# Kernel tuning notes

Measured on AMD Instinct MI355X. Metric: run time of the kernel, lower is better.

## Reference

```python
import jax, jax.numpy as jnp
import numpy as np

D_MODEL = 1024
NUM_HEADS = 16
D_INTERNAL = D_MODEL // NUM_HEADS
ROPE_BASE = 10000.0


def justnorm(x):
    return x / jnp.linalg.norm(x, axis=-1, keepdims=True)


def rotate_half(x):
    h = x.shape[-1] // 2
    return jnp.concatenate([-x[..., h:], x[..., :h]], axis=-1)


def setup_inputs() -> dict:
    key = jax.random.key(0)
    ks = jax.random.split(key, 8)
    B, T, dm, H, di = 4, 2048, D_MODEL, NUM_HEADS, D_INTERNAL
    x = jax.random.normal(ks[0], (B, T, dm), dtype=jnp.float32)
    stdev_h = 1.0 / (dm + di) ** 0.5
    qkv = jax.random.uniform(ks[1], (H, 3 * di, dm), minval=-stdev_h, maxval=stdev_h, dtype=jnp.float32)
    qkv = justnorm(qkv)  # per-row L2 normalization as in torch init
    sqk = (dm ** -0.5) * jnp.ones((H, di), dtype=jnp.float32)
    stdev = 1.0 / (4 * dm + dm) ** 0.5
    W_O = justnorm(jax.random.uniform(ks[2], (dm, dm), minval=-stdev, maxval=stdev, dtype=jnp.float32))
    Wu = justnorm(jax.random.uniform(ks[3], (8 * dm, dm), minval=-stdev, maxval=stdev, dtype=jnp.float32))
    Wv = justnorm(jax.random.uniform(ks[4], (dm, 4 * dm), minval=-stdev, maxval=stdev, dtype=jnp.float32))
    attn_alpha = (dm ** -0.5) * jnp.ones((dm,), dtype=jnp.float32)
    mlp_alpha = jnp.ones((dm,), dtype=jnp.float32)
    suv = jnp.ones((8 * dm,), dtype=jnp.float32)
    return {"x": x, "qkv": qkv, "sqk": sqk, "W_O": W_O, "Wu": Wu, "Wv": Wv,
            "attn_alpha": attn_alpha, "mlp_alpha": mlp_alpha, "suv": suv}


def _forward(x, qkv, sqk, W_O, Wu, Wv, attn_alpha, mlp_alpha, suv):
    B, T, dm = x.shape
    H = qkv.shape[0]
    di = qkv.shape[1] // 3
    sqrt_dm = jnp.sqrt(jnp.asarray(dm, x.dtype))
    # Per-head QKV projection, batched over heads: [B,H,T,3*di]
    qkv_out = jnp.einsum('btd,hed->bhte', x, qkv)
    Q, K, V = jnp.split(qkv_out, 3, axis=-1)
    # RoPE over full d_internal
    inv_freq = 1.0 / (ROPE_BASE ** (jnp.arange(0, di, 2, dtype=jnp.float32) / di))
    freqs = jnp.arange(T, dtype=jnp.float32)[:, None] * inv_freq[None, :]
    emb = jnp.concatenate([freqs, freqs], axis=-1)  # [T, di]
    cos, sin = jnp.cos(emb), jnp.sin(emb)
    Q = Q * cos + rotate_half(Q) * sin
    K = K * cos + rotate_half(K) * sin
    # sqk effective scale: sqk * (1.0 / d_model**-0.5)
    sqk_eff = sqk * sqrt_dm  # [H, di]
    Q = justnorm(Q) * sqk_eff[None, :, None, :]
    K = justnorm(K) * sqk_eff[None, :, None, :]
    # SDPA with non-standard scale = d_model**0.5, causal (eval mode)
    scores = jnp.einsum('bhqd,bhkd->bhqk', Q, K) * sqrt_dm
    causal = jnp.tril(jnp.ones((T, T), dtype=bool))
    scores = jnp.where(causal[None, None], scores, jnp.finfo(x.dtype).min)
    attn = jax.nn.softmax(scores, axis=-1)
    out = jnp.einsum('bhqk,bhkd->bhqd', attn, V)
    t = out.transpose(0, 2, 1, 3).reshape(B, T, dm)
    t = t @ W_O.T
    # nGPT-style attention lerp residual: attn_alpha * (0.05 / d_model**-0.5)
    lr = jnp.abs(attn_alpha * (0.05 * sqrt_dm))
    A = justnorm(x)
    Bn = justnorm(t)
    x1 = justnorm(A + lr * (Bn - A))
    # SwiGLU MLP
    uv = x1 @ Wu.T
    uv = (suv * sqrt_dm) * uv
    tn = justnorm(uv)
    u, v = jnp.split(tn, 2, axis=-1)
    res = u * jax.nn.silu(v)
    t = res @ Wv.T
    lr2 = jnp.abs(mlp_alpha * 0.05)
    A = justnorm(x1)
    Bn = justnorm(t)
    return justnorm(A + lr2 * (Bn - A))


def reference(x, qkv, sqk, W_O, Wu, Wv, attn_alpha, mlp_alpha, suv):
    return _forward(x, qkv, sqk, W_O, Wu, Wv, attn_alpha, mlp_alpha, suv)
```

## Files before the change

### kernel.cpp

```cpp
#include <hip/hip_runtime.h>
#include <hip/hip_bf16.h>


#define B_   4
#define T_   2048
#define DM   1024
#define H_   16
#define DI   64
#define NROW (B_ * T_)

using bf16 = __hip_bfloat16;
typedef __attribute__((ext_vector_type(8))) short bfrag;
typedef __attribute__((ext_vector_type(4))) float f4;

__device__ __forceinline__ void  stf(float* p, float v) { *p = v; }
__device__ __forceinline__ void  stf(bf16* p, float v)  { *p = __float2bfloat16(v); }

__device__ __forceinline__ unsigned short bfbits(float a) {
    bf16 h = __float2bfloat16(a);
    return __builtin_bit_cast(unsigned short, h);
}
__device__ __forceinline__ unsigned pk2(float a, float b) {
    return (unsigned)bfbits(a) | ((unsigned)bfbits(b) << 16);
}

__device__ __forceinline__ float wave_sum(float v) {
#pragma unroll
    for (int off = 32; off; off >>= 1) v += __shfl_xor(v, off, 64);
    return v;
}

__device__ __forceinline__ float block_sum(float v) {
    __shared__ float sm[4];
    int lane = threadIdx.x & 63, w = threadIdx.x >> 6;
    v = wave_sum(v);
    __syncthreads();
    if (lane == 0) sm[w] = v;
    __syncthreads();
    return sm[0] + sm[1] + sm[2] + sm[3];
}

typedef __attribute__((address_space(1))) const void g_void;
typedef __attribute__((address_space(3))) void l_void;
__device__ __forceinline__ void gl_lds(const void* g, void* l) {
    __builtin_amdgcn_global_load_lds((g_void*)g, (l_void*)l, 16, 0, 0);
}

__global__ __launch_bounds__(256)
void f32_to_bf16_k(const float* __restrict__ in, bf16* __restrict__ out, long n)
{
    long i = ((long)blockIdx.x * 256 + threadIdx.x) * 8;
    if (i >= n) return;
    float4 a = *(const float4*)(in + i);
    float4 b = *(const float4*)(in + i + 4);
    union { bfrag f; unsigned u[4]; } o;
    o.u[0] = pk2(a.x, a.y); o.u[1] = pk2(a.z, a.w);
    o.u[2] = pk2(b.x, b.y); o.u[3] = pk2(b.z, b.w);
    *(bfrag*)(out + i) = o.f;
}

template <typename TC>
__global__ __launch_bounds__(256)
void gemm_bf16(const bf16* __restrict__ A, const bf16* __restrict__ Bm,
               TC* __restrict__ C, int M, int N, int K)
{
    __shared__ bf16 lds[2][2][128 * 32];
    const int tid  = threadIdx.x;
    const int w    = tid >> 6, lane = tid & 63;
    const int g    = lane >> 4, c = lane & 15;
    const int m0   = blockIdx.y * 128, n0 = blockIdx.x * 128;
    const int wm   = w >> 1, wn = w & 1;

    const int srow = (lane >> 2);
    const int skc  = 8 * (lane & 3);

    f4 acc[4][4] = {{{0,0,0,0}}};

    const int NT = K >> 5;

#pragma unroll
    for (int q = 0; q < 2; q++) {
        int cidx = w * 2 + q;
        int row  = 16 * cidx + srow;
        gl_lds(A + (long)(m0 + row) * K + skc, &lds[0][0][cidx * 512]);
        gl_lds(Bm + (long)(n0 + row) * K + skc, &lds[0][1][cidx * 512]);
    }
    __syncthreads();

    for (int t = 0; t < NT; t++) {
        int cur = t & 1;
        if (t + 1 < NT) {
            int k0 = (t + 1) << 5;
#pragma unroll
            for (int q = 0; q < 2; q++) {
                int cidx = w * 2 + q;
                int row  = 16 * cidx + srow;
                gl_lds(A + (long)(m0 + row) * K + k0 + skc, &lds[cur ^ 1][0][cidx * 512]);
                gl_lds(Bm + (long)(n0 + row) * K + k0 + skc, &lds[cur ^ 1][1][cidx * 512]);
            }
        }
        const bf16* bufA = &lds[cur][0][0];
        const bf16* bufB = &lds[cur][1][0];
        bfrag af[4], bb[4];
#pragma unroll
        for (int mi = 0; mi < 4; mi++)
            af[mi] = *(const bfrag*)(bufA + (64 * wm + 16 * mi + c) * 32 + 8 * g);
#pragma unroll
        for (int ni = 0; ni < 4; ni++)
            bb[ni] = *(const bfrag*)(bufB + (64 * wn + 16 * ni + c) * 32 + 8 * g);
#pragma unroll
        for (int mi = 0; mi < 4; mi++)
#pragma unroll
            for (int ni = 0; ni < 4; ni++)
                acc[mi][ni] = __builtin_amdgcn_mfma_f32_16x16x32_bf16(
                    af[mi], bb[ni], acc[mi][ni], 0, 0, 0);
        __syncthreads();
    }

#pragma unroll
    for (int mi = 0; mi < 4; mi++)
#pragma unroll
        for (int ni = 0; ni < 4; ni++) {
            long row = m0 + 64 * wm + 16 * mi + 4 * g;
            long col = n0 + 64 * wn + 16 * ni + c;
#pragma unroll
            for (int r = 0; r < 4; r++)
                stf(&C[(row + r) * N + col], acc[mi][ni][r]);
        }
}

template <typename TC>
__global__ __launch_bounds__(512, 2)
void gemm_bf16_256(const bf16* __restrict__ A, const bf16* __restrict__ Bm,
                   TC* __restrict__ C, int M, int N, int K)
{
    __shared__ bf16 lds[2][2][256 * 64];
    const int tid  = threadIdx.x;
    const int w    = tid >> 6, lane = tid & 63;
    const int g    = lane >> 4, c = lane & 15;
    const int m0   = blockIdx.y * 256, n0 = blockIdx.x * 256;
    const int wm   = w & 1, wn = w >> 1;
    const int srow8 = lane >> 3;
    const int swz   = 8 * ((lane & 7) ^ srow8);
    const int cx    = c & 7;

    f4 acc[8][4] = {{{0,0,0,0}}};

    const int NT = K >> 6;

    auto STAGE = [&](int buf, int t) {
        int k0 = t << 6;
#pragma unroll
        for (int i = 0; i < 4; i++) {
            int rb = w * 32 + i * 8;
            gl_lds(A  + (long)(m0 + rb + srow8) * K + k0 + swz, &lds[buf][0][rb * 64]);
            gl_lds(Bm + (long)(n0 + rb + srow8) * K + k0 + swz, &lds[buf][1][rb * 64]);
        }
    };

    STAGE(0, 0);
    STAGE(1, 1);
    asm volatile("s_waitcnt vmcnt(8)" ::: "memory");
    __builtin_amdgcn_s_barrier();

    for (int t = 0; t < NT; t++) {
        const bf16* bufA = &lds[t & 1][0][0];
        const bf16* bufB = &lds[t & 1][1][0];

        bfrag a0[4][2], b0[4][2];
#pragma unroll
        for (int mi = 0; mi < 4; mi++)
#pragma unroll
            for (int kk = 0; kk < 2; kk++)
                a0[mi][kk] = *(const bfrag*)(bufA + (wm * 128 + mi * 16 + c) * 64
                                                  + 8 * ((4 * kk + g) ^ cx));
#pragma unroll
        for (int ni = 0; ni < 4; ni++)
#pragma unroll
            for (int kk = 0; kk < 2; kk++)
                b0[ni][kk] = *(const bfrag*)(bufB + (wn * 64 + ni * 16 + c) * 64
                                                  + 8 * ((4 * kk + g) ^ cx));
        asm volatile("s_waitcnt lgkmcnt(0)" ::: "memory");
        __builtin_amdgcn_sched_barrier(0);
        __builtin_amdgcn_s_setprio(1);
#pragma unroll
        for (int mi = 0; mi < 4; mi++)
#pragma unroll
            for (int ni = 0; ni < 4; ni++) {
                acc[mi][ni] = __builtin_amdgcn_mfma_f32_16x16x32_bf16(
                    a0[mi][0], b0[ni][0], acc[mi][ni], 0, 0, 0);
                acc[mi][ni] = __builtin_amdgcn_mfma_f32_16x16x32_bf16(
                    a0[mi][1], b0[ni][1], acc[mi][ni], 0, 0, 0);
            }
        __builtin_amdgcn_s_setprio(0);

        bfrag a1[4][2];
#pragma unroll
        for (int mi = 0; mi < 4; mi++)
#pragma unroll
            for (int kk = 0; kk < 2; kk++)
                a1[mi][kk] = *(const bfrag*)(bufA + (wm * 128 + (mi + 4) * 16 + c) * 64
                                                  + 8 * ((4 * kk + g) ^ cx));
        asm volatile("s_waitcnt lgkmcnt(0)" ::: "memory");
        __builtin_amdgcn_sched_barrier(0);
        __builtin_amdgcn_s_setprio(1);
#pragma unroll
        for (int mi = 0; mi < 4; mi++)
#pragma unroll
            for (int ni = 0; ni < 4; ni++) {
                acc[mi + 4][ni] = __builtin_amdgcn_mfma_f32_16x16x32_bf16(
                    a1[mi][0], b0[ni][0], acc[mi + 4][ni], 0, 0, 0);
                acc[mi + 4][ni] = __builtin_amdgcn_mfma_f32_16x16x32_bf16(
                    a1[mi][1], b0[ni][1], acc[mi + 4][ni], 0, 0, 0);
            }
        __builtin_amdgcn_s_setprio(0);

        __builtin_amdgcn_s_barrier();
        if (t + 2 < NT) {
            STAGE(t & 1, t + 2);
            asm volatile("s_waitcnt vmcnt(8)" ::: "memory");
        } else if (t + 1 < NT) {
            asm volatile("s_waitcnt vmcnt(0)" ::: "memory");
        }
        __builtin_amdgcn_s_barrier();
    }

#pragma unroll
    for (int mi = 0; mi < 8; mi++)
#pragma unroll
        for (int ni = 0; ni < 4; ni++) {
            long row = m0 + wm * 128 + mi * 16 + 4 * g;
            long col = n0 + wn * 64 + ni * 16 + c;
#pragma unroll
            for (int r = 0; r < 4; r++)
                stf(&C[(row + r) * N + col], acc[mi][ni][r]);
        }
}

__global__ __launch_bounds__(256)
void rope_norm_qk(const bf16* __restrict__ QKVb, const float* __restrict__ sqk,
                  bf16* __restrict__ Qb, bf16* __restrict__ Kb, bf16* __restrict__ Vt)
{
    int gw   = (blockIdx.x * 256 + threadIdx.x) >> 6;
    int lane = threadIdx.x & 63;
    int h = gw / NROW, row = gw % NROW, t = row % T_, b = row / T_;

    const bf16* base = QKVb + (long)row * 3072 + h * 192;
    float q = __bfloat162float(base[lane]);
    float k = __bfloat162float(base[64 + lane]);
    bf16  v = base[128 + lane];

    int   j   = lane & 31;
    float inv = expf(-(float)j * (9.210340371976184f / 32.f));
    float ang = (float)t * inv;
    float s = sinf(ang), cc = cosf(ang);

    float qp = __shfl_xor(q, 32, 64);
    float kp = __shfl_xor(k, 32, 64);
    float sgn = (lane < 32) ? -1.f : 1.f;
    float qr = q * cc + sgn * qp * s;
    float kr = k * cc + sgn * kp * s;

    float qs = wave_sum(qr * qr);
    float ks = wave_sum(kr * kr);
    float se = sqk[h * 64 + lane] * 32.f;

    long idx = ((long)h * NROW + row) * 64 + lane;
    Qb[idx] = __float2bfloat16(qr * rsqrtf(qs) * se * 32.f);
    Kb[idx] = __float2bfloat16(kr * rsqrtf(ks) * se);
    Vt[((long)(h * B_ + b) * 64 + lane) * T_ + t] = v;
}

__global__ __launch_bounds__(256)
void attn_mfma(const bf16* __restrict__ Qb, const bf16* __restrict__ Kb,
               const bf16* __restrict__ Vt, bf16* __restrict__ O)
{
    __shared__ bf16 kv[2][2][64 * 64];

    int orig   = blockIdx.x;
    int xcd    = orig & 7;
    int rest   = orig >> 3;
    int bh     = xcd * 8 + (rest & 7);
    int blkraw = rest >> 3;
    int blk    = (blkraw & 1) ? (15 - (blkraw >> 1)) : (blkraw >> 1);
    int w      = threadIdx.x >> 6;
    int pr     = blk * 4 + w;
    int h = bh >> 2, b = bh & 3;

    int lane = threadIdx.x & 63;
    int g = lane >> 4, c = lane & 15;

    const bf16* kbase = Kb + ((long)h * NROW + (long)b * T_) * 64;
    const bf16* vbase = Vt + (long)(h * B_ + b) * 64 * (long)T_;

    int q0A = pr * 16, q0B = (127 - pr) * 16;
    const bf16* qbA = Qb + ((long)h * NROW + (long)b * T_ + q0A) * 64;
    const bf16* qbB = Qb + ((long)h * NROW + (long)b * T_ + q0B) * 64;
    bfrag qfA0 = *(const bfrag*)(qbA + (long)c * 64 + 8 * g);
    bfrag qfA1 = *(const bfrag*)(qbA + (long)c * 64 + 32 + 8 * g);
    bfrag qfB0 = *(const bfrag*)(qbB + (long)c * 64 + 8 * g);
    bfrag qfB1 = *(const bfrag*)(qbB + (long)c * 64 + 32 + 8 * g);

    f4 otA[4] = {{0,0,0,0},{0,0,0,0},{0,0,0,0},{0,0,0,0}};
    f4 otB[4] = {{0,0,0,0},{0,0,0,0},{0,0,0,0},{0,0,0,0}};
    float lA = 0.f, lB = 0.f;

    const int nA = blk, nB = 31 - blk, KT = nB;
    int qgA = q0A + c, qgB = q0B + c;

    const int srow8  = lane >> 3;
    const int schunk = (lane & 7) ^ srow8;
    const int swz    = 8 * schunk;

    auto STAGE = [&](int buf, int kt) {
        int k0 = kt * 64;
#pragma unroll
        for (int i = 0; i < 2; i++) {
            int rb  = (w * 2 + i) * 8;
            int row = rb + srow8;
            gl_lds(kbase + (long)(k0 + row) * 64 + swz, &kv[buf][0][rb * 64]);
            gl_lds(vbase + (long)row * T_ + k0 + swz,   &kv[buf][1][rb * 64]);
        }
    };

    STAGE(0, 0);
    __syncthreads();

    const int cx = c & 7;

    for (int kt = 0; kt <= KT; kt++) {
        int buf = kt & 1;
        if (kt < KT) STAGE(buf ^ 1, kt + 1);

        const bf16* Kl = &kv[buf][0][0];
        const bf16* Vl = &kv[buf][1][0];
        int k0 = kt * 64;
        bool actA = (kt <= nA);
        unsigned wvA[8], wvB[8];

#pragma unroll
        for (int kb = 0; kb < 4; kb++) {
            const bf16* kr = Kl + (16 * kb + c) * 64;
            bfrag ka = *(const bfrag*)(kr + 8 * (g ^ cx));
            bfrag kc = *(const bfrag*)(kr + 8 * ((g | 4) ^ cx));

            f4 sB = {0, 0, 0, 0};
            sB = __builtin_amdgcn_mfma_f32_16x16x32_bf16(ka, qfB0, sB, 0, 0, 0);
            sB = __builtin_amdgcn_mfma_f32_16x16x32_bf16(kc, qfB1, sB, 0, 0, 0);
            if (kt == nB) {
#pragma unroll
                for (int r = 0; r < 4; r++)
                    if (k0 + 16 * kb + 4 * g + r > qgB) sB[r] = -1e30f;
            }
            float eB0 = __expf(sB[0] - 32.f), eB1 = __expf(sB[1] - 32.f);
            float eB2 = __expf(sB[2] - 32.f), eB3 = __expf(sB[3] - 32.f);
            lB += (eB0 + eB1) + (eB2 + eB3);
            wvB[2 * kb]     = pk2(eB0, eB1);
            wvB[2 * kb + 1] = pk2(eB2, eB3);

            if (actA) {
                f4 sA = {0, 0, 0, 0};
                sA = __builtin_amdgcn_mfma_f32_16x16x32_bf16(ka, qfA0, sA, 0, 0, 0);
                sA = __builtin_amdgcn_mfma_f32_16x16x32_bf16(kc, qfA1, sA, 0, 0, 0);
                if (kt == nA) {
#pragma unroll
                    for (int r = 0; r < 4; r++)
                        if (k0 + 16 * kb + 4 * g + r > qgA) sA[r] = -1e30f;
                }
                float eA0 = __expf(sA[0] - 32.f), eA1 = __expf(sA[1] - 32.f);
                float eA2 = __expf(sA[2] - 32.f), eA3 = __expf(sA[3] - 32.f);
                lA += (eA0 + eA1) + (eA2 + eA3);
                wvA[2 * kb]     = pk2(eA0, eA1);
                wvA[2 * kb + 1] = pk2(eA2, eA3);
            }
        }

#pragma unroll
        for (int p = 0; p < 2; p++) {
            int s0l = c + 32 * (g & 1), s1l = s0l + 16;
            bool hi = (g >= 2);

            unsigned Bb0 = (unsigned)__shfl((int)wvB[4 * p + 0], s0l, 64);
            unsigned Bb1 = (unsigned)__shfl((int)wvB[4 * p + 1], s0l, 64);
            unsigned Bb2 = (unsigned)__shfl((int)wvB[4 * p + 2], s0l, 64);
            unsigned Bb3 = (unsigned)__shfl((int)wvB[4 * p + 3], s0l, 64);
            unsigned Bb4 = (unsigned)__shfl((int)wvB[4 * p + 0], s1l, 64);
            unsigned Bb5 = (unsigned)__shfl((int)wvB[4 * p + 1], s1l, 64);
            unsigned Bb6 = (unsigned)__shfl((int)wvB[4 * p + 2], s1l, 64);
            unsigned Bb7 = (unsigned)__shfl((int)wvB[4 * p + 3], s1l, 64);
            union { bfrag f; unsigned u[4]; } pfB;
            pfB.u[0] = hi ? Bb2 : Bb0;
            pfB.u[1] = hi ? Bb3 : Bb1;
            pfB.u[2] = hi ? Bb6 : Bb4;
            pfB.u[3] = hi ? Bb7 : Bb5;

            union { bfrag f; unsigned u[4]; } pfA;
            if (actA) {
                unsigned Ab0 = (unsigned)__shfl((int)wvA[4 * p + 0], s0l, 64);
                unsigned Ab1 = (unsigned)__shfl((int)wvA[4 * p + 1], s0l, 64);
                unsigned Ab2 = (unsigned)__shfl((int)wvA[4 * p + 2], s0l, 64);
                unsigned Ab3 = (unsigned)__shfl((int)wvA[4 * p + 3], s0l, 64);
                unsigned Ab4 = (unsigned)__shfl((int)wvA[4 * p + 0], s1l, 64);
                unsigned Ab5 = (unsigned)__shfl((int)wvA[4 * p + 1], s1l, 64);
                unsigned Ab6 = (unsigned)__shfl((int)wvA[4 * p + 2], s1l, 64);
                unsigned Ab7 = (unsigned)__shfl((int)wvA[4 * p + 3], s1l, 64);
                pfA.u[0] = hi ? Ab2 : Ab0;
                pfA.u[1] = hi ? Ab3 : Ab1;
                pfA.u[2] = hi ? Ab6 : Ab4;
                pfA.u[3] = hi ? Ab7 : Ab5;
            }

#pragma unroll
            for (int dblk = 0; dblk < 4; dblk++) {
                bfrag vf = *(const bfrag*)(Vl + (16 * dblk + c) * 64
                                              + 8 * (((p << 2) | g) ^ cx));
                otB[dblk] = __builtin_amdgcn_mfma_f32_16x16x32_bf16(vf, pfB.f, otB[dblk], 0, 0, 0);
                if (actA)
                    otA[dblk] = __builtin_amdgcn_mfma_f32_16x16x32_bf16(vf, pfA.f, otA[dblk], 0, 0, 0);
            }
        }
        __syncthreads();
    }

    lA += __shfl_xor(lA, 16, 64); lA += __shfl_xor(lA, 32, 64);
    lB += __shfl_xor(lB, 16, 64); lB += __shfl_xor(lB, 32, 64);

    float invA = 1.f / lA, invB = 1.f / lB;
    long orowA = (long)(b * T_ + q0A + c) * DM + h * 64;
    long orowB = (long)(b * T_ + q0B + c) * DM + h * 64;
#pragma unroll
    for (int dblk = 0; dblk < 4; dblk++)
#pragma unroll
        for (int r = 0; r < 4; r++) {
            O[orowA + 16 * dblk + 4 * g + r] = __float2bfloat16(otA[dblk][r] * invA);
            O[orowB + 16 * dblk + 4 * g + r] = __float2bfloat16(otB[dblk][r] * invB);
        }
}

__global__ __launch_bounds__(256)
void lerp_norm(const float* __restrict__ X, const float* __restrict__ Tt,
               const float* __restrict__ alpha, float ascale,
               float* __restrict__ Out, bf16* __restrict__ OutB)
{
    long row = blockIdx.x;
    const float* xr = X  + row * DM;
    const float* tr = Tt + row * DM;
    int tid = threadIdx.x;

    float xs[4], ts[4], sx = 0.f, st = 0.f;
#pragma unroll
    for (int i = 0; i < 4; i++) {
        int d = tid + 256 * i;
        xs[i] = xr[d]; ts[i] = tr[d];
        sx += xs[i] * xs[i]; st += ts[i] * ts[i];
    }
    sx = block_sum(sx);
    st = block_sum(st);
    float ix = rsqrtf(sx), it = rsqrtf(st);

    float ys[4], sy = 0.f;
#pragma unroll
    for (int i = 0; i < 4; i++) {
        int d = tid + 256 * i;
        float a  = xs[i] * ix;
        float bn = ts[i] * it;
        float lr = fabsf(alpha[d] * ascale);
        ys[i] = a + lr * (bn - a);
        sy += ys[i] * ys[i];
    }
    sy = block_sum(sy);
    float iy = rsqrtf(sy);
#pragma unroll
    for (int i = 0; i < 4; i++) {
        int d = tid + 256 * i;
        float o = ys[i] * iy;
        Out[row * DM + d] = o;
        if (OutB) OutB[row * DM + d] = __float2bfloat16(o);
    }
}

__global__ __launch_bounds__(256)
void mlp_act(const bf16* __restrict__ UV, const float* __restrict__ suv,
             bf16* __restrict__ R)
{
    long row = blockIdx.x;
    const bf16* ur = UV + row * 8192;
    int tid = threadIdx.x;

    float ss = 0.f;
#pragma unroll
    for (int i = 0; i < 32; i++) {
        int j = tid + 256 * i;
        float v = __bfloat162float(ur[j]) * suv[j] * 32.f;
        ss += v * v;
    }
    ss = block_sum(ss);
    float inv = rsqrtf(ss);

#pragma unroll
    for (int i = 0; i < 16; i++) {
        int j = tid + 256 * i;
        float u = __bfloat162float(ur[j])        * suv[j]        * 32.f * inv;
        float v = __bfloat162float(ur[4096 + j]) * suv[4096 + j] * 32.f * inv;
        float sil = v / (1.f + __expf(-v));
        R[row * 4096 + j] = __float2bfloat16(u * sil);
    }
}

extern "C" void kernel_launch(void* const* d_in, const int* in_sizes, int n_in,
                              void* d_out, int out_size, void* d_ws, size_t ws_size,
                              hipStream_t stream)
{
    const float* x          = (const float*)d_in[0];
    const float* qkv_w      = (const float*)d_in[1];
    const float* sqk        = (const float*)d_in[2];
    const float* W_O        = (const float*)d_in[3];
    const float* Wu         = (const float*)d_in[4];
    const float* Wv         = (const float*)d_in[5];
    const float* attn_alpha = (const float*)d_in[6];
    const float* mlp_alpha  = (const float*)d_in[7];
    const float* suv        = (const float*)d_in[8];
    float* out = (float*)d_out;

    const long MiB = 1048576;
    char* ws = (char*)d_ws;
    float* x1    = (float*)(ws + 0 * MiB);
    bf16*  x1b   = (bf16*) (ws + 32 * MiB);
    bf16*  QKVb  = (bf16*) (ws + 48 * MiB);
    float* tbuf  = (float*)(ws + 48 * MiB);
    bf16*  uv    = (bf16*) (ws + 48 * MiB);
    float* t2    = (float*)(ws + 48 * MiB);
    bf16*  xb    = (bf16*) (ws + 144 * MiB);
    bf16*  Qb    = (bf16*) (ws + 144 * MiB);
    bf16*  Wub   = (bf16*) (ws + 144 * MiB);
    bf16*  Kb    = (bf16*) (ws + 160 * MiB);
    bf16*  Vt    = (bf16*) (ws + 176 * MiB);
    bf16*  Wvb   = (bf16*) (ws + 176 * MiB);
    bf16*  res   = (bf16*) (ws + 112 * MiB);
    bf16*  qkvwb = (bf16*) (ws + 192 * MiB);
    bf16*  attno = (bf16*) (ws + 192 * MiB);
    bf16*  Wob   = (bf16*) (ws + 208 * MiB);

    f32_to_bf16_k<<<4096, 256, 0, stream>>>(x, xb, 8388608L);
    f32_to_bf16_k<<<1536, 256, 0, stream>>>(qkv_w, qkvwb, 3145728L);
    f32_to_bf16_k<<<512,  256, 0, stream>>>(W_O, Wob, 1048576L);

    gemm_bf16_256<bf16><<<dim3(12, 32), 512, 0, stream>>>(xb, qkvwb, QKVb, NROW, 3072, DM);

    rope_norm_qk<<<(H_ * NROW) / 4, 256, 0, stream>>>(QKVb, sqk, Qb, Kb, Vt);

    attn_mfma<<<1024, 256, 0, stream>>>(Qb, Kb, Vt, attno);

    gemm_bf16<float><<<dim3(8, 64), 256, 0, stream>>>(attno, Wob, tbuf, NROW, DM, DM);

    lerp_norm<<<NROW, 256, 0, stream>>>(x, tbuf, attn_alpha, 1.6f, x1, x1b);

    f32_to_bf16_k<<<4096, 256, 0, stream>>>(Wu, Wub, 8388608L);
    f32_to_bf16_k<<<2048, 256, 0, stream>>>(Wv, Wvb, 4194304L);

    for (int half = 0; half < 2; half++) {
        gemm_bf16_256<bf16><<<dim3(32, 16), 512, 0, stream>>>(
            x1b + (long)half * 4096 * DM, Wub, uv, 4096, 8 * DM, DM);
        mlp_act<<<4096, 256, 0, stream>>>(uv, suv, res + (long)half * 4096 * 4096);
    }

    gemm_bf16<float><<<dim3(8, 64), 256, 0, stream>>>(res, Wvb, t2, NROW, DM, 4 * DM);

    lerp_norm<<<NROW, 256, 0, stream>>>(x1, t2, mlp_alpha, 0.05f, out, (bf16*)nullptr);
}
```

Before: 588.9 us.

## Use bf16 GEMM outputs, exp2 softmax with folded bias, and extra GEMM barriers

The two output-projection GEMMs now write bf16 instead of fp32, and lerp_norm is templated to read bf16. This halves the intermediate traffic. In attention, the softmax scale is folded into Q as a log2(e)-scaled factor and the max offset goes into the MFMA accumulator init, so the exponent becomes a bare exp2f. MFMA regions get setprio hints. The 256-tile GEMM gains extra s_barriers around its compute phases to keep waves in lockstep. These are several unrelated changes, and the bf16 intermediates lose some precision before normalization.

```diff
diff --git a/kernel.cpp b/kernel.cpp
--- a/kernel.cpp
+++ b/kernel.cpp
@@ -13,6 +13,10 @@
 typedef __attribute__((ext_vector_type(8))) short bfrag;
 typedef __attribute__((ext_vector_type(4))) float f4;
 
+#define EXPB 46.166241f
+
+__device__ __forceinline__ float ldf(const float* p) { return *p; }
+__device__ __forceinline__ float ldf(const bf16* p)  { return __bfloat162float(*p); }
 __device__ __forceinline__ void  stf(float* p, float v) { *p = v; }
 __device__ __forceinline__ void  stf(bf16* p, float v)  { *p = __float2bfloat16(v); }
 
@@ -180,6 +184,8 @@
             for (int kk = 0; kk < 2; kk++)
                 b0[ni][kk] = *(const bfrag*)(bufB + (wn * 64 + ni * 16 + c) * 64
                                                   + 8 * ((4 * kk + g) ^ cx));
+        __builtin_amdgcn_sched_barrier(0);
+        __builtin_amdgcn_s_barrier();
         asm volatile("s_waitcnt lgkmcnt(0)" ::: "memory");
         __builtin_amdgcn_sched_barrier(0);
         __builtin_amdgcn_s_setprio(1);
@@ -193,6 +199,7 @@
                     a0[mi][1], b0[ni][1], acc[mi][ni], 0, 0, 0);
             }
         __builtin_amdgcn_s_setprio(0);
+        __builtin_amdgcn_s_barrier();
 
         bfrag a1[4][2];
 #pragma unroll
@@ -214,8 +221,8 @@
                     a1[mi][1], b0[ni][1], acc[mi + 4][ni], 0, 0, 0);
             }
         __builtin_amdgcn_s_setprio(0);
-
         __builtin_amdgcn_s_barrier();
+
         if (t + 2 < NT) {
             STAGE(t & 1, t + 2);
             asm volatile("s_waitcnt vmcnt(8)" ::: "memory");
@@ -266,7 +273,7 @@
     float se = sqk[h * 64 + lane] * 32.f;
 
     long idx = ((long)h * NROW + row) * 64 + lane;
-    Qb[idx] = __float2bfloat16(qr * rsqrtf(qs) * se * 32.f);
+    Qb[idx] = __float2bfloat16(qr * rsqrtf(qs) * se * EXPB);
     Kb[idx] = __float2bfloat16(kr * rsqrtf(ks) * se);
     Vt[((long)(h * B_ + b) * 64 + lane) * T_ + t] = v;
 }
@@ -301,6 +308,8 @@
     bfrag qfB0 = *(const bfrag*)(qbB + (long)c * 64 + 8 * g);
     bfrag qfB1 = *(const bfrag*)(qbB + (long)c * 64 + 32 + 8 * g);
 
+    const f4 CINIT = {-EXPB, -EXPB, -EXPB, -EXPB};
+
     f4 otA[4] = {{0,0,0,0},{0,0,0,0},{0,0,0,0},{0,0,0,0}};
     f4 otB[4] = {{0,0,0,0},{0,0,0,0},{0,0,0,0},{0,0,0,0}};
     float lA = 0.f, lB = 0.f;
@@ -309,8 +318,7 @@
     int qgA = q0A + c, qgB = q0B + c;
 
     const int srow8  = lane >> 3;
-    const int schunk = (lane & 7) ^ srow8;
-    const int swz    = 8 * schunk;
+    const int swz    = 8 * ((lane & 7) ^ srow8);
 
     auto STAGE = [&](int buf, int kt) {
         int k0 = kt * 64;
@@ -344,31 +352,33 @@
             bfrag ka = *(const bfrag*)(kr + 8 * (g ^ cx));
             bfrag kc = *(const bfrag*)(kr + 8 * ((g | 4) ^ cx));
 
-            f4 sB = {0, 0, 0, 0};
-            sB = __builtin_amdgcn_mfma_f32_16x16x32_bf16(ka, qfB0, sB, 0, 0, 0);
+            __builtin_amdgcn_s_setprio(1);
+            f4 sB = __builtin_amdgcn_mfma_f32_16x16x32_bf16(ka, qfB0, CINIT, 0, 0, 0);
             sB = __builtin_amdgcn_mfma_f32_16x16x32_bf16(kc, qfB1, sB, 0, 0, 0);
+            __builtin_amdgcn_s_setprio(0);
             if (kt == nB) {
 #pragma unroll
                 for (int r = 0; r < 4; r++)
                     if (k0 + 16 * kb + 4 * g + r > qgB) sB[r] = -1e30f;
             }
-            float eB0 = __expf(sB[0] - 32.f), eB1 = __expf(sB[1] - 32.f);
-            float eB2 = __expf(sB[2] - 32.f), eB3 = __expf(sB[3] - 32.f);
+            float eB0 = exp2f(sB[0]), eB1 = exp2f(sB[1]);
+            float eB2 = exp2f(sB[2]), eB3 = exp2f(sB[3]);
             lB += (eB0 + eB1) + (eB2 + eB3);
             wvB[2 * kb]     = pk2(eB0, eB1);
             wvB[2 * kb + 1] = pk2(eB2, eB3);
 
             if (actA) {
-                f4 sA = {0, 0, 0, 0};
-                sA = __builtin_amdgcn_mfma_f32_16x16x32_bf16(ka, qfA0, sA, 0, 0, 0);
+                __builtin_amdgcn_s_setprio(1);
+                f4 sA = __builtin_amdgcn_mfma_f32_16x16x32_bf16(ka, qfA0, CINIT, 0, 0, 0);
                 sA = __builtin_amdgcn_mfma_f32_16x16x32_bf16(kc, qfA1, sA, 0, 0, 0);
+                __builtin_amdgcn_s_setprio(0);
                 if (kt == nA) {
 #pragma unroll
                     for (int r = 0; r < 4; r++)
                         if (k0 + 16 * kb + 4 * g + r > qgA) sA[r] = -1e30f;
                 }
-                float eA0 = __expf(sA[0] - 32.f), eA1 = __expf(sA[1] - 32.f);
-                float eA2 = __expf(sA[2] - 32.f), eA3 = __expf(sA[3] - 32.f);
+                float eA0 = exp2f(sA[0]), eA1 = exp2f(sA[1]);
+                float eA2 = exp2f(sA[2]), eA3 = exp2f(sA[3]);
                 lA += (eA0 + eA1) + (eA2 + eA3);
                 wvA[2 * kb]     = pk2(eA0, eA1);
                 wvA[2 * kb + 1] = pk2(eA2, eA3);
@@ -410,6 +420,7 @@
                 pfA.u[3] = hi ? Ab7 : Ab5;
             }
 
+            __builtin_amdgcn_s_setprio(1);
 #pragma unroll
             for (int dblk = 0; dblk < 4; dblk++) {
                 bfrag vf = *(const bfrag*)(Vl + (16 * dblk + c) * 64
@@ -418,6 +429,7 @@
                 if (actA)
                     otA[dblk] = __builtin_amdgcn_mfma_f32_16x16x32_bf16(vf, pfA.f, otA[dblk], 0, 0, 0);
             }
+            __builtin_amdgcn_s_setprio(0);
         }
         __syncthreads();
     }
@@ -437,21 +449,22 @@
         }
 }
 
+template <typename TT>
 __global__ __launch_bounds__(256)
-void lerp_norm(const float* __restrict__ X, const float* __restrict__ Tt,
+void lerp_norm(const float* __restrict__ X, const TT* __restrict__ Tt,
                const float* __restrict__ alpha, float ascale,
                float* __restrict__ Out, bf16* __restrict__ OutB)
 {
     long row = blockIdx.x;
     const float* xr = X  + row * DM;
-    const float* tr = Tt + row * DM;
+    const TT*    tr = Tt + row * DM;
     int tid = threadIdx.x;
 
     float xs[4], ts[4], sx = 0.f, st = 0.f;
 #pragma unroll
     for (int i = 0; i < 4; i++) {
         int d = tid + 256 * i;
-        xs[i] = xr[d]; ts[i] = tr[d];
+        xs[i] = xr[d]; ts[i] = ldf(&tr[d]);
         sx += xs[i] * xs[i]; st += ts[i] * ts[i];
     }
     sx = block_sum(sx);
@@ -527,9 +540,9 @@
     float* x1    = (float*)(ws + 0 * MiB);
     bf16*  x1b   = (bf16*) (ws + 32 * MiB);
     bf16*  QKVb  = (bf16*) (ws + 48 * MiB);
-    float* tbuf  = (float*)(ws + 48 * MiB);
+    bf16*  tbuf  = (bf16*) (ws + 48 * MiB);
     bf16*  uv    = (bf16*) (ws + 48 * MiB);
-    float* t2    = (float*)(ws + 48 * MiB);
+    bf16*  t2    = (bf16*) (ws + 48 * MiB);
     bf16*  xb    = (bf16*) (ws + 144 * MiB);
     bf16*  Qb    = (bf16*) (ws + 144 * MiB);
     bf16*  Wub   = (bf16*) (ws + 144 * MiB);
@@ -551,9 +564,9 @@
 
     attn_mfma<<<1024, 256, 0, stream>>>(Qb, Kb, Vt, attno);
 
-    gemm_bf16<float><<<dim3(8, 64), 256, 0, stream>>>(attno, Wob, tbuf, NROW, DM, DM);
-
-    lerp_norm<<<NROW, 256, 0, stream>>>(x, tbuf, attn_alpha, 1.6f, x1, x1b);
+    gemm_bf16<bf16><<<dim3(8, 64), 256, 0, stream>>>(attno, Wob, tbuf, NROW, DM, DM);
+
+    lerp_norm<bf16><<<NROW, 256, 0, stream>>>(x, tbuf, attn_alpha, 1.6f, x1, x1b);
 
     f32_to_bf16_k<<<4096, 256, 0, stream>>>(Wu, Wub, 8388608L);
     f32_to_bf16_k<<<2048, 256, 0, stream>>>(Wv, Wvb, 4194304L);
@@ -564,7 +577,7 @@
         mlp_act<<<4096, 256, 0, stream>>>(uv, suv, res + (long)half * 4096 * 4096);
     }
 
-    gemm_bf16<float><<<dim3(8, 64), 256, 0, stream>>>(res, Wvb, t2, NROW, DM, 4 * DM);
-
-    lerp_norm<<<NROW, 256, 0, stream>>>(x1, t2, mlp_alpha, 0.05f, out, (bf16*)nullptr);
-}
+    gemm_bf16<bf16><<<dim3(8, 64), 256, 0, stream>>>(res, Wvb, t2, NROW, DM, 4 * DM);
+
+    lerp_norm<bf16><<<NROW, 256, 0, stream>>>(x1, t2, mlp_alpha, 0.05f, out, (bf16*)nullptr);
+}
```

After: 607.1 us. +3.1%, slower.
